# Optimization experiments

Hardware: AMD Instinct MI355X
Metric: run time of the kernel (lower is better)

Reference implementation:

```python
import jax, jax.numpy as jnp
import numpy as np

E = 16      # num_experts
H = 1024    # hidden_size
O = 1       # output_size
B = 4096    # batch
K = 2       # top-k (hard-coded in module)


def setup_inputs() -> dict:
    key = jax.random.key(0)
    ks = jax.random.split(key, 7)
    s_h = 1.0 / np.sqrt(H)
    inp = {
        "embeddings": jax.random.normal(ks[0], (B, H), dtype=jnp.float32),
        "router_w": jax.random.uniform(ks[1], (H, E), jnp.float32, -s_h, s_h),
        "router_b": jax.random.uniform(ks[2], (E,), jnp.float32, -s_h, s_h),
        "w1": jax.random.uniform(ks[3], (E, H, H), jnp.float32, -s_h, s_h),
        "b1": jax.random.uniform(ks[4], (E, H), jnp.float32, -s_h, s_h),
        "w2": jax.random.uniform(ks[5], (E, H, O), jnp.float32, -s_h, s_h),
        "b2": jax.random.uniform(ks[6], (E, O), jnp.float32, -s_h, s_h),
    }
    return inp


def reference(embeddings, router_w, router_b, w1, b1, w2, b2):
    # Router: top-2 experts per token, softmax over the 2 selected logits.
    logits = embeddings @ router_w + router_b                 # [B, E]
    top_vals, top_idx = jax.lax.top_k(logits, K)              # [B, K]
    top_w = jax.nn.softmax(top_vals, axis=-1)                 # [B, K]

    # Per-expert combine weight: w_e[b] = sum_k top_w[b,k] * (top_idx[b,k]==e)
    onehot = (top_idx[:, :, None] == jnp.arange(E)[None, None, :])  # [B, K, E]
    comb = jnp.einsum('bk,bke->eb', top_w, onehot.astype(top_w.dtype))  # [E, B]

    # Dense per-expert 2-layer MLP (small fixed E); masked-weighted combine
    # reproduces the gather/scatter-add exactly.
    h = jax.nn.relu(jnp.einsum('bh,ehd->ebd', embeddings, w1) + b1[:, None, :])  # [E, B, H]
    out = jnp.einsum('ebd,edo->ebo', h, w2) + b2[:, None, :]                      # [E, B, O]
    prediction = jnp.einsum('eb,ebo->bo', comb, out)                              # [B, O]
    return prediction
```

## Files before the change

kernel.cpp:

```cpp
#include <hip/hip_runtime.h>
#include <hip/hip_bf16.h>
#include <stdint.h>

#define E_EXP 16
#define H_DIM 1024
#define B_TOK 4096
#define BK 64
#define GBM 128
#define GBN 64
#define NSLOT 32
#define KS 16
#define KC 64
#define RTM 128
#define RSTRIDE (KC + 4)

typedef short bf16x8 __attribute__((ext_vector_type(8)));
typedef float f32x4 __attribute__((ext_vector_type(4)));

__device__ __forceinline__ unsigned short f2bf(float x) {
  union { float f; unsigned u; } v; v.f = x;
  unsigned r = v.u + 0x7FFFu + ((v.u >> 16) & 1u);
  return (unsigned short)(r >> 16);
}

__device__ __forceinline__ void gload_lds16(const void* g, void* l) {
  __builtin_amdgcn_global_load_lds(
      (const __attribute__((address_space(1))) void*)g,
      (__attribute__((address_space(3))) void*)l, 16, 0, 0);
}

__global__ __launch_bounds__(256) void k_router_gemm(
    const float* __restrict__ emb, const float* __restrict__ rw,
    unsigned short* __restrict__ emb_bf, float* __restrict__ part)
{
  __shared__ float embL[RTM * RSTRIDE];
  __shared__ float rwL[KC * E_EXP];

  const int t0 = blockIdx.x * RTM;
  const int ks = blockIdx.y;
  const int tid = threadIdx.x;

#pragma unroll
  for (int it = 0; it < 8; ++it) {
    const int i = tid + 256 * it;
    const int row = i >> 4;
    const int c4 = i & 15;
    const size_t goff = (size_t)(t0 + row) * H_DIM + ks * KC + c4 * 4;
    const f32x4 v = *(const f32x4*)(emb + goff);
    ushort4 o;
    o.x = f2bf(v[0]); o.y = f2bf(v[1]); o.z = f2bf(v[2]); o.w = f2bf(v[3]);
    *(ushort4*)(emb_bf + goff) = o;
    *(f32x4*)(embL + row * RSTRIDE + c4 * 4) = v;
  }
  {
    const f32x4 v = *(const f32x4*)(rw + (size_t)ks * (KC * E_EXP) + tid * 4);
    *(f32x4*)(rwL + tid * 4) = v;
  }
  __syncthreads();

  const int w = tid >> 6, lane = tid & 63;
  const int tg = lane & 15, eg = lane >> 4;
  const int ta = w * 32 + tg, tb = ta + 16;

  f32x4 accA = {0.f, 0.f, 0.f, 0.f};
  f32x4 accB = {0.f, 0.f, 0.f, 0.f};
#pragma unroll
  for (int k4 = 0; k4 < KC / 4; ++k4) {
    const f32x4 e0 = *(const f32x4*)(embL + ta * RSTRIDE + k4 * 4);
    const f32x4 e1 = *(const f32x4*)(embL + tb * RSTRIDE + k4 * 4);
#pragma unroll
    for (int h = 0; h < 4; ++h) {
      const f32x4 r = *(const f32x4*)(rwL + (k4 * 4 + h) * E_EXP + eg * 4);
      accA += e0[h] * r;
      accB += e1[h] * r;
    }
  }

  *(f32x4*)(part + ((size_t)ks * B_TOK + t0 + ta) * E_EXP + eg * 4) = accA;
  *(f32x4*)(part + ((size_t)ks * B_TOK + t0 + tb) * E_EXP + eg * 4) = accB;
}

__global__ __launch_bounds__(256) void k_router_select(
    const float* __restrict__ part, const float* __restrict__ rb,
    int* __restrict__ counts, int* __restrict__ lists,
    int4* __restrict__ meta, float2* __restrict__ wts)
{
  __shared__ int lcnt[E_EXP];
  __shared__ int base[E_EXP];
  const int tid = threadIdx.x;
  const int t = blockIdx.x * 256 + tid;
  if (tid < E_EXP) lcnt[tid] = 0;

  float lg[16];
#pragma unroll
  for (int q = 0; q < 4; ++q) {
    const f32x4 b = *(const f32x4*)(rb + q * 4);
    lg[q * 4 + 0] = b[0]; lg[q * 4 + 1] = b[1];
    lg[q * 4 + 2] = b[2]; lg[q * 4 + 3] = b[3];
  }
#pragma unroll
  for (int s = 0; s < KS; ++s) {
#pragma unroll
    for (int q = 0; q < 4; ++q) {
      const f32x4 v = *(const f32x4*)(part + ((size_t)s * B_TOK + t) * E_EXP + q * 4);
      lg[q * 4 + 0] += v[0]; lg[q * 4 + 1] += v[1];
      lg[q * 4 + 2] += v[2]; lg[q * 4 + 3] += v[3];
    }
  }

  float best = -1e30f; int b0 = 0;
#pragma unroll
  for (int e = 0; e < 16; ++e)
    if (lg[e] > best) { best = lg[e]; b0 = e; }
  float best2 = -1e30f; int b1i = 0;
#pragma unroll
  for (int e = 0; e < 16; ++e)
    if (e != b0 && lg[e] > best2) { best2 = lg[e]; b1i = e; }

  __syncthreads();
  const int l0 = atomicAdd(&lcnt[b0], 1);
  const int l1 = atomicAdd(&lcnt[b1i], 1);
  __syncthreads();
  if (tid < E_EXP) base[tid] = atomicAdd(&counts[tid], lcnt[tid]);
  __syncthreads();

  const int p0 = base[b0] + l0;
  const int p1 = base[b1i] + l1;
  lists[b0 * B_TOK + p0] = t;
  lists[b1i * B_TOK + p1] = t;
  meta[t] = make_int4(b0, b1i, p0, p1);
  const float e1v = expf(best2 - best);
  const float w0 = 1.f / (1.f + e1v);
  wts[t] = make_float2(w0, e1v * w0);
}

__global__ __launch_bounds__(256) void k_w1t(const float* __restrict__ w1,
                                             unsigned short* __restrict__ w1t)
{
  __shared__ unsigned short tile[64][65];
  const int e = blockIdx.z;
  const int ht = blockIdx.x, dt = blockIdx.y;
  const float* src = w1 + ((size_t)e * H_DIM + ht * 64) * H_DIM + dt * 64;
  const int tr = threadIdx.x >> 4;
  const int tc = threadIdx.x & 15;
#pragma unroll
  for (int i = 0; i < 4; ++i) {
    const int r = tr + i * 16;
    const float4 v = *(const float4*)(src + (size_t)r * H_DIM + tc * 4);
    tile[r][tc * 4 + 0] = f2bf(v.x);
    tile[r][tc * 4 + 1] = f2bf(v.y);
    tile[r][tc * 4 + 2] = f2bf(v.z);
    tile[r][tc * 4 + 3] = f2bf(v.w);
  }
  __syncthreads();
  unsigned short* dst = w1t + ((size_t)e * H_DIM + dt * 64) * H_DIM + ht * 64;
  const int wr = threadIdx.x >> 3;
  const int wc = threadIdx.x & 7;
#pragma unroll
  for (int i = 0; i < 2; ++i) {
    const int r = wr + i * 32;
    ushort4 t0, t1;
    t0.x = tile[wc * 8 + 0][r]; t0.y = tile[wc * 8 + 1][r];
    t0.z = tile[wc * 8 + 2][r]; t0.w = tile[wc * 8 + 3][r];
    t1.x = tile[wc * 8 + 4][r]; t1.y = tile[wc * 8 + 5][r];
    t1.z = tile[wc * 8 + 6][r]; t1.w = tile[wc * 8 + 7][r];
    *(ushort4*)(dst + (size_t)r * H_DIM + wc * 8) = t0;
    *(ushort4*)(dst + (size_t)r * H_DIM + wc * 8 + 4) = t1;
  }
}

__global__ __launch_bounds__(256, 4) void k_moe_gemm(
    const unsigned short* __restrict__ emb_bf,
    const unsigned short* __restrict__ w1t,
    const float* __restrict__ b1, const float* __restrict__ w2,
    const int* __restrict__ counts, const int* __restrict__ lists,
    float* __restrict__ outbuf)
{
  const int bid = blockIdx.x;
  const int xcd = bid & 7;
  const int j = bid >> 3;
  const int e  = xcd + 8 * (j >> 7);
  const int r  = j & 127;
  const int nb = r >> 3;
  const int mbg = r & 7;
  const int cnt = counts[e];

  __shared__ unsigned short lA[GBM * BK];
  __shared__ unsigned short lB[GBN * BK];
  __shared__ int toks[GBM];

  const int tid = threadIdx.x;
  const int w = tid >> 6, lane = tid & 63;
  const int scb = ((lane & 7) * 16) ^ ((lane >> 3) << 4);
  const int wm = w >> 1, wn = w & 1;
  const int lr = lane & 15, lg = lane >> 4;

  const unsigned short* w1tb = w1t + ((size_t)e * H_DIM + nb * GBN) * H_DIM;
  const float* b1e = b1 + (size_t)e * H_DIM + nb * GBN;
  const float* w2e = w2 + (size_t)e * H_DIM + nb * GBN;

  const unsigned short* bSrc[2];
#pragma unroll
  for (int i = 0; i < 2; ++i) {
    const int n = (w * 2 + i) * 8 + (lane >> 3);
    bSrc[i] = w1tb + (size_t)n * H_DIM + (scb >> 1);
  }

  for (int mb = mbg; mb * GBM < cnt; mb += 8) {
    if (tid < GBM) {
      const int p = mb * GBM + tid;
      toks[tid] = lists[e * B_TOK + (p < cnt ? p : 0)];
    }
    __syncthreads();

    const unsigned short* aSrc[4];
#pragma unroll
    for (int i = 0; i < 4; ++i) {
      const int row = (w * 4 + i) * 8 + (lane >> 3);
      aSrc[i] = emb_bf + (size_t)toks[row] * H_DIM + (scb >> 1);
    }

    f32x4 acc[4][2];
#pragma unroll
    for (int m = 0; m < 4; ++m)
#pragma unroll
      for (int n = 0; n < 2; ++n) acc[m][n] = (f32x4){0.f, 0.f, 0.f, 0.f};

    for (int k0 = 0; k0 < H_DIM; k0 += BK) {
#pragma unroll
      for (int i = 0; i < 4; ++i)
        gload_lds16(aSrc[i] + k0, (char*)lA + (w * 4 + i) * 1024);
#pragma unroll
      for (int i = 0; i < 2; ++i)
        gload_lds16(bSrc[i] + k0, (char*)lB + (w * 2 + i) * 1024);
      __syncthreads();

#pragma unroll
      for (int kk = 0; kk < 2; ++kk) {
        const int kb = kk * 64 + lg * 16;
        bf16x8 af[4], bfr[2];
#pragma unroll
        for (int m = 0; m < 4; ++m) {
          const int row = wm * 64 + m * 16 + lr;
          af[m] = *(const bf16x8*)((const char*)lA + row * 128 + (kb ^ ((row & 7) << 4)));
        }
#pragma unroll
        for (int n = 0; n < 2; ++n) {
          const int row = wn * 32 + n * 16 + lr;
          bfr[n] = *(const bf16x8*)((const char*)lB + row * 128 + (kb ^ ((row & 7) << 4)));
        }
        __builtin_amdgcn_s_setprio(1);
#pragma unroll
        for (int m = 0; m < 4; ++m)
#pragma unroll
          for (int n = 0; n < 2; ++n)
            acc[m][n] = __builtin_amdgcn_mfma_f32_16x16x32_bf16(af[m], bfr[n], acc[m][n], 0, 0, 0);
        __builtin_amdgcn_s_setprio(0);
      }
      __syncthreads();
    }

    float rs[4][4];
#pragma unroll
    for (int m = 0; m < 4; ++m)
#pragma unroll
      for (int r4 = 0; r4 < 4; ++r4) rs[m][r4] = 0.f;

#pragma unroll
    for (int n = 0; n < 2; ++n) {
      const int d = wn * 32 + n * 16 + lr;
      const float bb = b1e[d];
      const float ww = w2e[d];
#pragma unroll
      for (int m = 0; m < 4; ++m)
#pragma unroll
        for (int r4 = 0; r4 < 4; ++r4) {
          float v = acc[m][n][r4] + bb;
          v = fmaxf(v, 0.f);
          rs[m][r4] = fmaf(v, ww, rs[m][r4]);
        }
    }
#pragma unroll
    for (int mask = 8; mask >= 1; mask >>= 1) {
#pragma unroll
      for (int m = 0; m < 4; ++m)
#pragma unroll
        for (int r4 = 0; r4 < 4; ++r4) rs[m][r4] += __shfl_xor(rs[m][r4], mask, 64);
    }

    if (lr == 0) {
      const int slot = nb * 2 + wn;
      float* ob = outbuf + ((size_t)slot * E_EXP + e) * B_TOK + mb * GBM;
#pragma unroll
      for (int m = 0; m < 4; ++m)
#pragma unroll
        for (int r4 = 0; r4 < 4; ++r4)
          ob[wm * 64 + m * 16 + lg * 4 + r4] = rs[m][r4];
    }
    __syncthreads();
  }
}

__global__ __launch_bounds__(256) void k_combine(
    const int4* __restrict__ meta, const float2* __restrict__ wts,
    const float* __restrict__ outbuf, const float* __restrict__ b2,
    float* __restrict__ out)
{
  const int t = blockIdx.x * 256 + threadIdx.x;
  if (t >= B_TOK) return;
  const int4 m = meta[t];
  const float2 w = wts[t];
  float o0 = b2[m.x], o1 = b2[m.y];
#pragma unroll
  for (int s = 0; s < NSLOT; ++s) {
    o0 += outbuf[((size_t)s * E_EXP + m.x) * B_TOK + m.z];
    o1 += outbuf[((size_t)s * E_EXP + m.y) * B_TOK + m.w];
  }
  out[t] = w.x * o0 + w.y * o1;
}

extern "C" void kernel_launch(void* const* d_in, const int* in_sizes, int n_in,
                              void* d_out, int out_size, void* d_ws, size_t ws_size,
                              hipStream_t stream)
{
  const float* emb = (const float*)d_in[0];
  const float* rw  = (const float*)d_in[1];
  const float* rb  = (const float*)d_in[2];
  const float* w1  = (const float*)d_in[3];
  const float* b1  = (const float*)d_in[4];
  const float* w2  = (const float*)d_in[5];
  const float* b2  = (const float*)d_in[6];
  float* out = (float*)d_out;

  char* ws = (char*)d_ws;
  size_t cur = 0;
  auto alloc = [&](size_t bytes) -> void* {
    void* p = ws + cur;
    cur += (bytes + 255) & ~(size_t)255;
    return p;
  };
  int*            counts = (int*)alloc(64);
  int4*           meta   = (int4*)alloc((size_t)B_TOK * 16);
  float2*         wts    = (float2*)alloc((size_t)B_TOK * 8);
  int*            lists  = (int*)alloc((size_t)E_EXP * B_TOK * 4);
  float*          outbuf = (float*)alloc((size_t)NSLOT * E_EXP * B_TOK * 4);
  float*          part   = (float*)alloc((size_t)KS * B_TOK * E_EXP * 4);
  unsigned short* emb_bf = (unsigned short*)alloc((size_t)B_TOK * H_DIM * 2);
  unsigned short* w1t    = (unsigned short*)alloc((size_t)E_EXP * H_DIM * H_DIM * 2);

  hipMemsetAsync(counts, 0, 64, stream);
  k_router_gemm<<<dim3(B_TOK / RTM, KS), 256, 0, stream>>>(emb, rw, emb_bf, part);
  k_router_select<<<B_TOK / 256, 256, 0, stream>>>(part, rb, counts, lists, meta, wts);
  k_w1t<<<dim3(16, 16, 16), 256, 0, stream>>>(w1, w1t);
  k_moe_gemm<<<dim3(2048), 256, 0, stream>>>(emb_bf, w1t, b1, w2, counts, lists, outbuf);
  k_combine<<<B_TOK / 256, 256, 0, stream>>>(meta, wts, outbuf, b2, out);
}
```

Baseline: 88.32 us.

## Fuse router GEMM with W1 transpose and double-buffer MoE GEMM k-loop

```diff
diff --git a/kernel.cpp b/kernel.cpp
--- a/kernel.cpp
+++ b/kernel.cpp
@@ -29,55 +29,92 @@
       (__attribute__((address_space(3))) void*)l, 16, 0, 0);
 }
 
-__global__ __launch_bounds__(256) void k_router_gemm(
+__global__ __launch_bounds__(256) void k_prep(
     const float* __restrict__ emb, const float* __restrict__ rw,
-    unsigned short* __restrict__ emb_bf, float* __restrict__ part)
-{
-  __shared__ float embL[RTM * RSTRIDE];
-  __shared__ float rwL[KC * E_EXP];
-
-  const int t0 = blockIdx.x * RTM;
-  const int ks = blockIdx.y;
+    const float* __restrict__ w1, unsigned short* __restrict__ emb_bf,
+    float* __restrict__ part, unsigned short* __restrict__ w1t)
+{
+  __shared__ __align__(16) char smem[RTM * RSTRIDE * 4 + KC * E_EXP * 4];
   const int tid = threadIdx.x;
 
-#pragma unroll
-  for (int it = 0; it < 8; ++it) {
-    const int i = tid + 256 * it;
-    const int row = i >> 4;
-    const int c4 = i & 15;
-    const size_t goff = (size_t)(t0 + row) * H_DIM + ks * KC + c4 * 4;
-    const f32x4 v = *(const f32x4*)(emb + goff);
-    ushort4 o;
-    o.x = f2bf(v[0]); o.y = f2bf(v[1]); o.z = f2bf(v[2]); o.w = f2bf(v[3]);
-    *(ushort4*)(emb_bf + goff) = o;
-    *(f32x4*)(embL + row * RSTRIDE + c4 * 4) = v;
-  }
-  {
-    const f32x4 v = *(const f32x4*)(rw + (size_t)ks * (KC * E_EXP) + tid * 4);
-    *(f32x4*)(rwL + tid * 4) = v;
-  }
-  __syncthreads();
-
-  const int w = tid >> 6, lane = tid & 63;
-  const int tg = lane & 15, eg = lane >> 4;
-  const int ta = w * 32 + tg, tb = ta + 16;
-
-  f32x4 accA = {0.f, 0.f, 0.f, 0.f};
-  f32x4 accB = {0.f, 0.f, 0.f, 0.f};
-#pragma unroll
-  for (int k4 = 0; k4 < KC / 4; ++k4) {
-    const f32x4 e0 = *(const f32x4*)(embL + ta * RSTRIDE + k4 * 4);
-    const f32x4 e1 = *(const f32x4*)(embL + tb * RSTRIDE + k4 * 4);
-#pragma unroll
-    for (int h = 0; h < 4; ++h) {
-      const f32x4 r = *(const f32x4*)(rwL + (k4 * 4 + h) * E_EXP + eg * 4);
-      accA += e0[h] * r;
-      accB += e1[h] * r;
-    }
-  }
-
-  *(f32x4*)(part + ((size_t)ks * B_TOK + t0 + ta) * E_EXP + eg * 4) = accA;
-  *(f32x4*)(part + ((size_t)ks * B_TOK + t0 + tb) * E_EXP + eg * 4) = accB;
+  if (blockIdx.x < 512) {
+    float* embL = (float*)smem;
+    float* rwL  = (float*)(smem + RTM * RSTRIDE * 4);
+    const int t0 = (blockIdx.x & 31) * RTM;
+    const int ks = blockIdx.x >> 5;
+
+#pragma unroll
+    for (int it = 0; it < 8; ++it) {
+      const int i = tid + 256 * it;
+      const int row = i >> 4;
+      const int c4 = i & 15;
+      const size_t goff = (size_t)(t0 + row) * H_DIM + ks * KC + c4 * 4;
+      const f32x4 v = *(const f32x4*)(emb + goff);
+      ushort4 o;
+      o.x = f2bf(v[0]); o.y = f2bf(v[1]); o.z = f2bf(v[2]); o.w = f2bf(v[3]);
+      *(ushort4*)(emb_bf + goff) = o;
+      *(f32x4*)(embL + row * RSTRIDE + c4 * 4) = v;
+    }
+    {
+      const f32x4 v = *(const f32x4*)(rw + (size_t)ks * (KC * E_EXP) + tid * 4);
+      *(f32x4*)(rwL + tid * 4) = v;
+    }
+    __syncthreads();
+
+    const int w = tid >> 6, lane = tid & 63;
+    const int tg = lane & 15, eg = lane >> 4;
+    const int ta = w * 32 + tg, tb = ta + 16;
+
+    f32x4 accA = {0.f, 0.f, 0.f, 0.f};
+    f32x4 accB = {0.f, 0.f, 0.f, 0.f};
+#pragma unroll
+    for (int k4 = 0; k4 < KC / 4; ++k4) {
+      const f32x4 e0 = *(const f32x4*)(embL + ta * RSTRIDE + k4 * 4);
+      const f32x4 e1 = *(const f32x4*)(embL + tb * RSTRIDE + k4 * 4);
+#pragma unroll
+      for (int h = 0; h < 4; ++h) {
+        const f32x4 r = *(const f32x4*)(rwL + (k4 * 4 + h) * E_EXP + eg * 4);
+        accA += e0[h] * r;
+        accB += e1[h] * r;
+      }
+    }
+    *(f32x4*)(part + ((size_t)ks * B_TOK + t0 + ta) * E_EXP + eg * 4) = accA;
+    *(f32x4*)(part + ((size_t)ks * B_TOK + t0 + tb) * E_EXP + eg * 4) = accB;
+  } else {
+    typedef unsigned short TileT[65];
+    TileT* tile = (TileT*)smem;
+    const int wb = blockIdx.x - 512;
+    const int e  = wb >> 8;
+    const int ht = (wb >> 4) & 15;
+    const int dt = wb & 15;
+    const float* src = w1 + ((size_t)e * H_DIM + ht * 64) * H_DIM + dt * 64;
+    const int tr = tid >> 4;
+    const int tc = tid & 15;
+#pragma unroll
+    for (int i = 0; i < 4; ++i) {
+      const int r = tr + i * 16;
+      const float4 v = *(const float4*)(src + (size_t)r * H_DIM + tc * 4);
+      tile[r][tc * 4 + 0] = f2bf(v.x);
+      tile[r][tc * 4 + 1] = f2bf(v.y);
+      tile[r][tc * 4 + 2] = f2bf(v.z);
+      tile[r][tc * 4 + 3] = f2bf(v.w);
+    }
+    __syncthreads();
+    unsigned short* dst = w1t + ((size_t)e * H_DIM + dt * 64) * H_DIM + ht * 64;
+    const int wr = tid >> 3;
+    const int wc = tid & 7;
+#pragma unroll
+    for (int i = 0; i < 2; ++i) {
+      const int r = wr + i * 32;
+      ushort4 t0, t1;
+      t0.x = tile[wc * 8 + 0][r]; t0.y = tile[wc * 8 + 1][r];
+      t0.z = tile[wc * 8 + 2][r]; t0.w = tile[wc * 8 + 3][r];
+      t1.x = tile[wc * 8 + 4][r]; t1.y = tile[wc * 8 + 5][r];
+      t1.z = tile[wc * 8 + 6][r]; t1.w = tile[wc * 8 + 7][r];
+      *(ushort4*)(dst + (size_t)r * H_DIM + wc * 8) = t0;
+      *(ushort4*)(dst + (size_t)r * H_DIM + wc * 8 + 4) = t1;
+    }
+  }
 }
 
 __global__ __launch_bounds__(256) void k_router_select(
@@ -134,42 +171,7 @@
   wts[t] = make_float2(w0, e1v * w0);
 }
 
-__global__ __launch_bounds__(256) void k_w1t(const float* __restrict__ w1,
-                                             unsigned short* __restrict__ w1t)
-{
-  __shared__ unsigned short tile[64][65];
-  const int e = blockIdx.z;
-  const int ht = blockIdx.x, dt = blockIdx.y;
-  const float* src = w1 + ((size_t)e * H_DIM + ht * 64) * H_DIM + dt * 64;
-  const int tr = threadIdx.x >> 4;
-  const int tc = threadIdx.x & 15;
-#pragma unroll
-  for (int i = 0; i < 4; ++i) {
-    const int r = tr + i * 16;
-    const float4 v = *(const float4*)(src + (size_t)r * H_DIM + tc * 4);
-    tile[r][tc * 4 + 0] = f2bf(v.x);
-    tile[r][tc * 4 + 1] = f2bf(v.y);
-    tile[r][tc * 4 + 2] = f2bf(v.z);
-    tile[r][tc * 4 + 3] = f2bf(v.w);
-  }
-  __syncthreads();
-  unsigned short* dst = w1t + ((size_t)e * H_DIM + dt * 64) * H_DIM + ht * 64;
-  const int wr = threadIdx.x >> 3;
-  const int wc = threadIdx.x & 7;
-#pragma unroll
-  for (int i = 0; i < 2; ++i) {
-    const int r = wr + i * 32;
-    ushort4 t0, t1;
-    t0.x = tile[wc * 8 + 0][r]; t0.y = tile[wc * 8 + 1][r];
-    t0.z = tile[wc * 8 + 2][r]; t0.w = tile[wc * 8 + 3][r];
-    t1.x = tile[wc * 8 + 4][r]; t1.y = tile[wc * 8 + 5][r];
-    t1.z = tile[wc * 8 + 6][r]; t1.w = tile[wc * 8 + 7][r];
-    *(ushort4*)(dst + (size_t)r * H_DIM + wc * 8) = t0;
-    *(ushort4*)(dst + (size_t)r * H_DIM + wc * 8 + 4) = t1;
-  }
-}
-
-__global__ __launch_bounds__(256, 4) void k_moe_gemm(
+__global__ __launch_bounds__(256, 3) void k_moe_gemm(
     const unsigned short* __restrict__ emb_bf,
     const unsigned short* __restrict__ w1t,
     const float* __restrict__ b1, const float* __restrict__ w2,
@@ -178,15 +180,15 @@
 {
   const int bid = blockIdx.x;
   const int xcd = bid & 7;
-  const int j = bid >> 3;
-  const int e  = xcd + 8 * (j >> 7);
-  const int r  = j & 127;
-  const int nb = r >> 3;
-  const int mbg = r & 7;
+  const int q   = bid >> 3;
+  const int e   = xcd + 8 * (q >> 6);
+  const int rr  = q & 63;
+  const int nb  = rr >> 2;
+  const int mbg = rr & 3;
   const int cnt = counts[e];
 
-  __shared__ unsigned short lA[GBM * BK];
-  __shared__ unsigned short lB[GBN * BK];
+  __shared__ unsigned short lA[2][GBM * BK];
+  __shared__ unsigned short lB[2][GBN * BK];
   __shared__ int toks[GBM];
 
   const int tid = threadIdx.x;
@@ -206,7 +208,7 @@
     bSrc[i] = w1tb + (size_t)n * H_DIM + (scb >> 1);
   }
 
-  for (int mb = mbg; mb * GBM < cnt; mb += 8) {
+  for (int mb = mbg; mb * GBM < cnt; mb += 4) {
     if (tid < GBM) {
       const int p = mb * GBM + tid;
       toks[tid] = lists[e * B_TOK + (p < cnt ? p : 0)];
@@ -226,15 +228,16 @@
 #pragma unroll
       for (int n = 0; n < 2; ++n) acc[m][n] = (f32x4){0.f, 0.f, 0.f, 0.f};
 
-    for (int k0 = 0; k0 < H_DIM; k0 += BK) {
+    auto stage = [&](int buf, int k0) {
 #pragma unroll
       for (int i = 0; i < 4; ++i)
-        gload_lds16(aSrc[i] + k0, (char*)lA + (w * 4 + i) * 1024);
+        gload_lds16(aSrc[i] + k0, (char*)lA[buf] + (w * 4 + i) * 1024);
 #pragma unroll
       for (int i = 0; i < 2; ++i)
-        gload_lds16(bSrc[i] + k0, (char*)lB + (w * 2 + i) * 1024);
-      __syncthreads();
-
+        gload_lds16(bSrc[i] + k0, (char*)lB[buf] + (w * 2 + i) * 1024);
+    };
+
+    auto compute = [&](int buf) {
 #pragma unroll
       for (int kk = 0; kk < 2; ++kk) {
         const int kb = kk * 64 + lg * 16;
@@ -242,12 +245,12 @@
 #pragma unroll
         for (int m = 0; m < 4; ++m) {
           const int row = wm * 64 + m * 16 + lr;
-          af[m] = *(const bf16x8*)((const char*)lA + row * 128 + (kb ^ ((row & 7) << 4)));
+          af[m] = *(const bf16x8*)((const char*)lA[buf] + row * 128 + (kb ^ ((row & 7) << 4)));
         }
 #pragma unroll
         for (int n = 0; n < 2; ++n) {
           const int row = wn * 32 + n * 16 + lr;
-          bfr[n] = *(const bf16x8*)((const char*)lB + row * 128 + (kb ^ ((row & 7) << 4)));
+          bfr[n] = *(const bf16x8*)((const char*)lB[buf] + row * 128 + (kb ^ ((row & 7) << 4)));
         }
         __builtin_amdgcn_s_setprio(1);
 #pragma unroll
@@ -257,8 +260,20 @@
             acc[m][n] = __builtin_amdgcn_mfma_f32_16x16x32_bf16(af[m], bfr[n], acc[m][n], 0, 0, 0);
         __builtin_amdgcn_s_setprio(0);
       }
+    };
+
+    stage(0, 0);
+    __syncthreads();
+
+    int cur = 0;
+#pragma unroll 1
+    for (int t = 0; t < H_DIM / BK - 1; ++t) {
+      stage(cur ^ 1, (t + 1) * BK);
+      compute(cur);
       __syncthreads();
-    }
+      cur ^= 1;
+    }
+    compute(cur);
 
     float rs[4][4];
 #pragma unroll
@@ -349,9 +364,8 @@
   unsigned short* w1t    = (unsigned short*)alloc((size_t)E_EXP * H_DIM * H_DIM * 2);
 
   hipMemsetAsync(counts, 0, 64, stream);
-  k_router_gemm<<<dim3(B_TOK / RTM, KS), 256, 0, stream>>>(emb, rw, emb_bf, part);
+  k_prep<<<dim3(512 + 4096), 256, 0, stream>>>(emb, rw, w1, emb_bf, part, w1t);
   k_router_select<<<B_TOK / 256, 256, 0, stream>>>(part, rb, counts, lists, meta, wts);
-  k_w1t<<<dim3(16, 16, 16), 256, 0, stream>>>(w1, w1t);
-  k_moe_gemm<<<dim3(2048), 256, 0, stream>>>(emb_bf, w1t, b1, w2, counts, lists, outbuf);
+  k_moe_gemm<<<dim3(1024), 256, 0, stream>>>(emb_bf, w1t, b1, w2, counts, lists, outbuf);
   k_combine<<<B_TOK / 256, 256, 0, stream>>>(meta, wts, outbuf, b2, out);
 }
```

After: 102.5 us. +16.1%, slower.

## Fuse w1 bf16 conversion and transpose into the MoE GEMM B-tile load

Applied to the files above, without the earlier changes.

```diff
diff --git a/kernel.cpp b/kernel.cpp
--- a/kernel.cpp
+++ b/kernel.cpp
@@ -134,44 +134,9 @@
   wts[t] = make_float2(w0, e1v * w0);
 }
 
-__global__ __launch_bounds__(256) void k_w1t(const float* __restrict__ w1,
-                                             unsigned short* __restrict__ w1t)
-{
-  __shared__ unsigned short tile[64][65];
-  const int e = blockIdx.z;
-  const int ht = blockIdx.x, dt = blockIdx.y;
-  const float* src = w1 + ((size_t)e * H_DIM + ht * 64) * H_DIM + dt * 64;
-  const int tr = threadIdx.x >> 4;
-  const int tc = threadIdx.x & 15;
-#pragma unroll
-  for (int i = 0; i < 4; ++i) {
-    const int r = tr + i * 16;
-    const float4 v = *(const float4*)(src + (size_t)r * H_DIM + tc * 4);
-    tile[r][tc * 4 + 0] = f2bf(v.x);
-    tile[r][tc * 4 + 1] = f2bf(v.y);
-    tile[r][tc * 4 + 2] = f2bf(v.z);
-    tile[r][tc * 4 + 3] = f2bf(v.w);
-  }
-  __syncthreads();
-  unsigned short* dst = w1t + ((size_t)e * H_DIM + dt * 64) * H_DIM + ht * 64;
-  const int wr = threadIdx.x >> 3;
-  const int wc = threadIdx.x & 7;
-#pragma unroll
-  for (int i = 0; i < 2; ++i) {
-    const int r = wr + i * 32;
-    ushort4 t0, t1;
-    t0.x = tile[wc * 8 + 0][r]; t0.y = tile[wc * 8 + 1][r];
-    t0.z = tile[wc * 8 + 2][r]; t0.w = tile[wc * 8 + 3][r];
-    t1.x = tile[wc * 8 + 4][r]; t1.y = tile[wc * 8 + 5][r];
-    t1.z = tile[wc * 8 + 6][r]; t1.w = tile[wc * 8 + 7][r];
-    *(ushort4*)(dst + (size_t)r * H_DIM + wc * 8) = t0;
-    *(ushort4*)(dst + (size_t)r * H_DIM + wc * 8 + 4) = t1;
-  }
-}
-
 __global__ __launch_bounds__(256, 4) void k_moe_gemm(
     const unsigned short* __restrict__ emb_bf,
-    const unsigned short* __restrict__ w1t,
+    const float* __restrict__ w1,
     const float* __restrict__ b1, const float* __restrict__ w2,
     const int* __restrict__ counts, const int* __restrict__ lists,
     float* __restrict__ outbuf)
@@ -195,16 +160,15 @@
   const int wm = w >> 1, wn = w & 1;
   const int lr = lane & 15, lg = lane >> 4;
 
-  const unsigned short* w1tb = w1t + ((size_t)e * H_DIM + nb * GBN) * H_DIM;
+  const int np  = tid & 31;
+  const int oct = tid >> 5;
+  const int row0 = 2 * np, row1 = 2 * np + 1;
+  const int wb0 = row0 * 128 + ((oct * 16) ^ ((row0 & 7) << 4));
+  const int wb1 = row1 * 128 + ((oct * 16) ^ ((row1 & 7) << 4));
+
+  const float* w1e = w1 + (size_t)e * H_DIM * H_DIM + nb * GBN + np * 2;
   const float* b1e = b1 + (size_t)e * H_DIM + nb * GBN;
   const float* w2e = w2 + (size_t)e * H_DIM + nb * GBN;
-
-  const unsigned short* bSrc[2];
-#pragma unroll
-  for (int i = 0; i < 2; ++i) {
-    const int n = (w * 2 + i) * 8 + (lane >> 3);
-    bSrc[i] = w1tb + (size_t)n * H_DIM + (scb >> 1);
-  }
 
   for (int mb = mbg; mb * GBM < cnt; mb += 8) {
     if (tid < GBM) {
@@ -230,9 +194,24 @@
 #pragma unroll
       for (int i = 0; i < 4; ++i)
         gload_lds16(aSrc[i] + k0, (char*)lA + (w * 4 + i) * 1024);
-#pragma unroll
-      for (int i = 0; i < 2; ++i)
-        gload_lds16(bSrc[i] + k0, (char*)lB + (w * 2 + i) * 1024);
+
+      {
+        const float* src = w1e + (size_t)(k0 + oct * 8) * H_DIM;
+        float lo[8], hi[8];
+#pragma unroll
+        for (int jj = 0; jj < 8; ++jj) {
+          const float2 v = *(const float2*)(src + (size_t)jj * H_DIM);
+          lo[jj] = v.x; hi[jj] = v.y;
+        }
+        union { unsigned short u[8]; bf16x8 v; } p0, p1;
+#pragma unroll
+        for (int jj = 0; jj < 8; ++jj) {
+          p0.u[jj] = f2bf(lo[jj]);
+          p1.u[jj] = f2bf(hi[jj]);
+        }
+        *(bf16x8*)((char*)lB + wb0) = p0.v;
+        *(bf16x8*)((char*)lB + wb1) = p1.v;
+      }
       __syncthreads();
 
 #pragma unroll
@@ -346,12 +325,10 @@
   float*          outbuf = (float*)alloc((size_t)NSLOT * E_EXP * B_TOK * 4);
   float*          part   = (float*)alloc((size_t)KS * B_TOK * E_EXP * 4);
   unsigned short* emb_bf = (unsigned short*)alloc((size_t)B_TOK * H_DIM * 2);
-  unsigned short* w1t    = (unsigned short*)alloc((size_t)E_EXP * H_DIM * H_DIM * 2);
 
   hipMemsetAsync(counts, 0, 64, stream);
   k_router_gemm<<<dim3(B_TOK / RTM, KS), 256, 0, stream>>>(emb, rw, emb_bf, part);
   k_router_select<<<B_TOK / 256, 256, 0, stream>>>(part, rb, counts, lists, meta, wts);
-  k_w1t<<<dim3(16, 16, 16), 256, 0, stream>>>(w1, w1t);
-  k_moe_gemm<<<dim3(2048), 256, 0, stream>>>(emb_bf, w1t, b1, w2, counts, lists, outbuf);
+  k_moe_gemm<<<dim3(2048), 256, 0, stream>>>(emb_bf, w1, b1, w2, counts, lists, outbuf);
   k_combine<<<B_TOK / 256, 256, 0, stream>>>(meta, wts, outbuf, b2, out);
 }
```

Result: slower. 98.85 us (+11.9%).
